# Performance work log

Measured on AMD Instinct MI355X. Metric: run time of the kernel, lower is better.

Reference implementation:

```python
import jax, jax.numpy as jnp
import numpy as np

NUM_LAYERS = 2
HIDDEN = 512


def setup_inputs() -> dict:
    key = jax.random.key(0)
    ks = jax.random.split(key, 5)
    B, T, D, L, H = 32, 512, 512, NUM_LAYERS, HIDDEN
    s = 1.0 / np.sqrt(H)
    return {
        "x": jax.random.normal(ks[0], (B, T, D), dtype=jnp.float32),
        "h0": jnp.zeros((B, L, H), dtype=jnp.float32),
        "c0": jnp.zeros((B, L, H), dtype=jnp.float32),
        "Wx": jax.random.normal(ks[1], (L, 4 * H, D), dtype=jnp.float32) * s,
        "bx": jax.random.normal(ks[2], (L, 4 * H), dtype=jnp.float32) * s,
        "Wh": jax.random.normal(ks[3], (L, 4 * H, H), dtype=jnp.float32) * s,
        "bh": jax.random.normal(ks[4], (L, 4 * H), dtype=jnp.float32) * s,
    }


def _lstm_forward(x, h0, c0, Wx, bx, Wh, bh):
    # x: [B,T,D]; h0,c0: [B,L,H]; Wx/Wh: [L,4H,*]; gate order (i,f,g,o)
    L, H = Wx.shape[0], Wx.shape[2]

    def step(carry, x_t):
        h, c = carry  # [B,L,H]
        inp = x_t  # [B,D]
        new_h, new_c = [], []
        for l in range(L):
            gates = (inp @ Wx[l].T + bx[l]) + (h[:, l] @ Wh[l].T + bh[l])  # [B,4H]
            i_g, f_g, g_g, o_g = jnp.split(gates, 4, axis=-1)
            c_l = jax.nn.sigmoid(f_g) * c[:, l] + jax.nn.sigmoid(i_g) * jnp.tanh(g_g)
            h_l = jax.nn.sigmoid(o_g) * jnp.tanh(c_l)
            new_h.append(h_l)
            new_c.append(c_l)
            inp = h_l
        return (jnp.stack(new_h, axis=1), jnp.stack(new_c, axis=1)), inp

    (h_n, c_n), ys = jax.lax.scan(step, (h0, c0), jnp.swapaxes(x, 0, 1))
    output = jnp.swapaxes(ys, 0, 1)  # [B,T,H]
    # torch module returns h_n/c_n swapped to [num_layers, batch, hidden]
    return output, (jnp.swapaxes(h_n, 0, 1), jnp.swapaxes(c_n, 0, 1))


def reference(x, h0, c0, Wx, bx, Wh, bh):
    return _lstm_forward(x, h0, c0, Wx, bx, Wh, bh)
```

## Files before the change

### kernel.cpp

```cpp
#include <hip/hip_runtime.h>
#include <hip/hip_bf16.h>

typedef __bf16 bf16x8 __attribute__((ext_vector_type(8)));
typedef float f32x4 __attribute__((ext_vector_type(4)));
typedef unsigned long long u64;

#define MFMA16(a, b, c) __builtin_amdgcn_mfma_f32_16x16x32_bf16((a), (b), (c), 0, 0, 0)

#define HN_OFF 8388608ull
#define CN_OFF 8421376ull

__device__ __forceinline__ float sigf(float x) { return 1.0f / (1.0f + __expf(-x)); }
__device__ __forceinline__ float b2f(unsigned short u) {
    union { unsigned u; float f; } c; c.u = ((unsigned)u) << 16; return c.f;
}
__device__ __forceinline__ unsigned short f2u(float f) {
    __hip_bfloat16 h = __float2bfloat16(f); return *(unsigned short*)&h;
}

__device__ __forceinline__ u64 gload8(const void* p) {
    return __hip_atomic_load((const u64*)p, __ATOMIC_RELAXED, __HIP_MEMORY_SCOPE_AGENT);
}
__device__ __forceinline__ void gstore8(void* p, u64 v) {
    __hip_atomic_store((u64*)p, v, __ATOMIC_RELAXED, __HIP_MEMORY_SCOPE_AGENT);
}

__device__ __forceinline__ void split8(const float* p, bf16x8& hi, bf16x8& lo) {
    union { __hip_bfloat16 h[8]; bf16x8 v; } uh, ul;
    #pragma unroll
    for (int i = 0; i < 8; ++i) {
        __hip_bfloat16 e = __float2bfloat16(p[i]);
        uh.h[i] = e;
        ul.h[i] = __float2bfloat16(p[i] - __bfloat162float(e));
    }
    hi = uh.v; lo = ul.v;
}

__global__ __launch_bounds__(256) void lstm_detect(
    const unsigned* __restrict__ Wq, unsigned* __restrict__ dflag,
    unsigned* __restrict__ flags)
{
    for (int j = threadIdx.x; j < 1024; j += 256) flags[j] = 0;
    if (threadIdx.x < 64) {
        int lane = threadIdx.x;
        int bad = 0;
        #pragma unroll
        for (int i = 0; i < 4; ++i) {
            unsigned u = Wq[(size_t)(lane + i * 64) * 4093];
            float v = b2f((unsigned short)(u & 0xFFFFu));
            if (!(v == v) || fabsf(v) > 100.0f) ++bad;
        }
        #pragma unroll
        for (int off = 32; off; off >>= 1) bad += __shfl_down(bad, off, 64);
        if (lane == 0) *dflag = (bad > 32) ? 1u : 0u;
    }
}

__global__ __launch_bounds__(256) void lstm_init(
    const void* __restrict__ h0v, const void* __restrict__ c0v,
    unsigned* __restrict__ h0p, unsigned* __restrict__ h1p,
    float* __restrict__ cws, const unsigned* __restrict__ dflag)
{
    const bool f32 = (*dflag != 0);
    int i = blockIdx.x * 256 + threadIdx.x;
    int b = i >> 9, n = i & 511;
    float f0, f1, g0, g1;
    if (f32) {
        const float* h = (const float*)h0v; const float* c = (const float*)c0v;
        f0 = h[(b * 2 + 0) * 512 + n];  f1 = h[(b * 2 + 1) * 512 + n];
        g0 = c[(b * 2 + 0) * 512 + n];  g1 = c[(b * 2 + 1) * 512 + n];
    } else {
        const unsigned short* h = (const unsigned short*)h0v;
        const unsigned short* c = (const unsigned short*)c0v;
        f0 = b2f(h[(b * 2 + 0) * 512 + n]);  f1 = b2f(h[(b * 2 + 1) * 512 + n]);
        g0 = b2f(c[(b * 2 + 0) * 512 + n]);  g1 = b2f(c[(b * 2 + 1) * 512 + n]);
    }
    unsigned short h0h = f2u(f0), h1h = f2u(f1);
    unsigned short h0l = f2u(f0 - b2f(h0h)), h1l = f2u(f1 - b2f(h1h));
    h0p[i] = ((unsigned)h0h << 16) | ((unsigned)h0l & 0xFFF0u) | 15u;
    h1p[i] = ((unsigned)h1h << 16) | ((unsigned)h1l & 0xFFF0u) | 0u;
    cws[i] = g0;  cws[16384 + i] = g1;
}

__global__ __launch_bounds__(256, 1) void lstm_seq(
    const void* __restrict__ xv,
    const void* __restrict__ Wxv, const void* __restrict__ bxv,
    const void* __restrict__ Whv, const void* __restrict__ bhv,
    unsigned* __restrict__ h0p, unsigned* __restrict__ h1p,
    const float* __restrict__ cws, unsigned* __restrict__ flags,
    const unsigned* __restrict__ dflag, void* __restrict__ outv)
{
    const bool f32 = (*dflag != 0);
    const int p  = blockIdx.x & 1;
    const int wt = blockIdx.x >> 1;
    const int tid = threadIdx.x;
    const int q = tid >> 6, lane = tid & 63;
    const int n16 = lane & 15, quad = lane >> 4;
    const int colg = q * 512 + wt * 16 + n16;

    __shared__ __align__(16) char smem[131072];
    __shared__ float gbuf[2176];

    float* outf = (float*)outv;
    __hip_bfloat16* outh = (__hip_bfloat16*)outv;

    bf16x8 wa[16], wal[16], wr[16], wrl[16];
    if (f32) {
        const float* WA = (const float*)Wxv + ((size_t)(p * 2048 + colg)) * 512;
        const float* WR = (const float*)Whv + ((size_t)(p * 2048 + colg)) * 512;
        #pragma unroll
        for (int kk = 0; kk < 16; ++kk) {
            split8(WA + kk * 32 + quad * 8, wa[kk], wal[kk]);
            split8(WR + kk * 32 + quad * 8, wr[kk], wrl[kk]);
        }
    } else {
        const unsigned short* WA = (const unsigned short*)Wxv + ((size_t)(p * 2048 + colg)) * 512;
        const unsigned short* WR = (const unsigned short*)Whv + ((size_t)(p * 2048 + colg)) * 512;
        union { uint4 u; bf16x8 v; } cvu;
        #pragma unroll
        for (int kk = 0; kk < 16; ++kk) {
            cvu.u = *(const uint4*)(WA + kk * 32 + quad * 8); wa[kk] = cvu.v;
            cvu.u = *(const uint4*)(WR + kk * 32 + quad * 8); wr[kk] = cvu.v;
        }
    }
    float bias;
    if (f32) bias = ((const float*)bxv)[p * 2048 + colg] + ((const float*)bhv)[p * 2048 + colg];
    else     bias = b2f(((const unsigned short*)bxv)[p * 2048 + colg])
                  + b2f(((const unsigned short*)bhv)[p * 2048 + colg]);

    const int e0 = tid * 2;
    const int pbb = e0 >> 4;
    const int pn0 = e0 & 15;
    float cv[2];
    cv[0] = cws[p * 16384 + pbb * 512 + wt * 16 + pn0];
    cv[1] = cws[p * 16384 + pbb * 512 + wt * 16 + pn0 + 1];

    const unsigned short* xb = (const unsigned short*)xv;

    #define STAGE_X_BF16(T)                                                      \
        { _Pragma("unroll")                                                      \
          for (int j = 0; j < 8; ++j) {                                          \
              int L = j * 256 + tid;                                             \
              int rem = L & 127;                                                 \
              int row = ((rem >> 6) << 4) + (rem & 15);                          \
              int kcol = ((L >> 7) << 5) + (((rem >> 4) & 3) << 3);              \
              *(uint4*)(smem + (L << 4)) =                                       \
                  *(const uint4*)(xb + ((size_t)row * 512 + (T)) * 512 + kcol);  \
          } }

    #define STAGE_X_F32(T)                                                       \
        { _Pragma("unroll")                                                      \
          for (int j = 0; j < 8; ++j) {                                          \
              int L = j * 256 + tid;                                             \
              int rem = L & 127;                                                 \
              int row = ((rem >> 6) << 4) + (rem & 15);                          \
              int kcol = ((L >> 7) << 5) + (((rem >> 4) & 3) << 3);              \
              const float* xp = (const float*)xv + ((size_t)row * 512 + (T)) * 512 + kcol; \
              bf16x8 hi_, lo_;                                                   \
              split8(xp, hi_, lo_);                                              \
              *(bf16x8*)(smem + (L << 4)) = hi_;                                 \
              *(bf16x8*)(smem + 32768 + (L << 4)) = lo_;                         \
          } }

    #define EOFF(S_) ({ int L_ = ((S_) >> 2) * 256 + tid; int rem_ = L_ & 127;    \
        int row_ = ((rem_ >> 6) << 4) + (rem_ & 15);                              \
        int kc_  = ((L_ >> 7) << 5) + (((rem_ >> 4) & 3) << 3);                   \
        row_ * 512 + kc_ + ((S_) & 3) * 2; })

    #define GISSUE(SRC)                                                           \
        { _Pragma("unroll")                                                       \
          for (int s_ = 0; s_ < 32; ++s_) V[s_] = gload8((const unsigned*)(SRC) + EOFF(s_)); }

    #define GCHECK(SRC, WANTV)                                                    \
        { const u64 WV_ = (u64)(WANTV) * 0x0000000100000001ULL;                   \
          for (;;) {                                                              \
              u64 d_ = 0;                                                         \
              _Pragma("unroll")                                                   \
              for (int s_ = 0; s_ < 32; ++s_)                                     \
                  d_ |= (V[s_] ^ WV_) & 0x0000000F0000000FULL;                    \
              if (d_ == 0) break;                                                 \
              __builtin_amdgcn_s_sleep(1);                                        \
              _Pragma("unroll")                                                   \
              for (int s_ = 0; s_ < 32; ++s_)                                     \
                  V[s_] = gload8((const unsigned*)(SRC) + EOFF(s_));              \
          } }

    #define GSCATTER(DH, DL)                                                      \
        { _Pragma("unroll")                                                       \
          for (int j_ = 0; j_ < 8; ++j_) {                                        \
              union { u64 q; unsigned w[2]; } a_, b_, c_, d_;                     \
              a_.q = V[j_*4+0]; b_.q = V[j_*4+1]; c_.q = V[j_*4+2]; d_.q = V[j_*4+3]; \
              uint4 hi_, lo_;                                                     \
              hi_.x = (a_.w[0] >> 16) | (a_.w[1] & 0xFFFF0000u);                  \
              hi_.y = (b_.w[0] >> 16) | (b_.w[1] & 0xFFFF0000u);                  \
              hi_.z = (c_.w[0] >> 16) | (c_.w[1] & 0xFFFF0000u);                  \
              hi_.w = (d_.w[0] >> 16) | (d_.w[1] & 0xFFFF0000u);                  \
              lo_.x = (a_.w[0] & 0xFFF0u) | ((a_.w[1] & 0xFFF0u) << 16);          \
              lo_.y = (b_.w[0] & 0xFFF0u) | ((b_.w[1] & 0xFFF0u) << 16);          \
              lo_.z = (c_.w[0] & 0xFFF0u) | ((c_.w[1] & 0xFFF0u) << 16);          \
              lo_.w = (d_.w[0] & 0xFFF0u) | ((d_.w[1] & 0xFFF0u) << 16);          \
              int L_ = j_ * 256 + tid;                                            \
              *(uint4*)(smem + (DH) + (L_ << 4)) = hi_;                           \
              *(uint4*)(smem + (DL) + (L_ << 4)) = lo_;                           \
          } }

    #define MM_A_F32()                                                           \
        { _Pragma("unroll")                                                      \
          for (int kk = 0; kk < 16; ++kk) {                                      \
              bf16x8 Aha = *(const bf16x8*)(sl + kk * 2048);                     \
              bf16x8 Ahb = *(const bf16x8*)(sl + kk * 2048 + 1024);              \
              bf16x8 Ala = *(const bf16x8*)(sl + 32768 + kk * 2048);             \
              bf16x8 Alb = *(const bf16x8*)(sl + 32768 + kk * 2048 + 1024);      \
              acc0 = MFMA16(Aha, wa[kk], acc0);  acc1 = MFMA16(Ahb, wa[kk], acc1);   \
              acc0 = MFMA16(Aha, wal[kk], acc0); acc1 = MFMA16(Ahb, wal[kk], acc1);  \
              acc0 = MFMA16(Ala, wa[kk], acc0);  acc1 = MFMA16(Alb, wa[kk], acc1);   \
          } }

    #define MM_R_F32()                                                           \
        { _Pragma("unroll")                                                      \
          for (int kk = 0; kk < 16; ++kk) {                                      \
              bf16x8 Rha = *(const bf16x8*)(sl + 65536 + kk * 2048);             \
              bf16x8 Rhb = *(const bf16x8*)(sl + 65536 + kk * 2048 + 1024);      \
              bf16x8 Rla = *(const bf16x8*)(sl + 98304 + kk * 2048);             \
              bf16x8 Rlb = *(const bf16x8*)(sl + 98304 + kk * 2048 + 1024);      \
              acc0 = MFMA16(Rha, wr[kk], acc0);  acc1 = MFMA16(Rhb, wr[kk], acc1);   \
              acc0 = MFMA16(Rha, wrl[kk], acc0); acc1 = MFMA16(Rhb, wrl[kk], acc1);  \
              acc0 = MFMA16(Rla, wr[kk], acc0);  acc1 = MFMA16(Rlb, wr[kk], acc1);   \
          } }

    #define MM_A_BF16_P0()                                                       \
        { _Pragma("unroll")                                                      \
          for (int kk = 0; kk < 16; ++kk) {                                      \
              bf16x8 Aha = *(const bf16x8*)(sl + kk * 2048);                     \
              bf16x8 Ahb = *(const bf16x8*)(sl + kk * 2048 + 1024);              \
              acc0 = MFMA16(Aha, wa[kk], acc0);  acc1 = MFMA16(Ahb, wa[kk], acc1);   \
          } }

    #define MM_A_BF16_P1()                                                       \
        { _Pragma("unroll")                                                      \
          for (int kk = 0; kk < 16; ++kk) {                                      \
              bf16x8 Aha = *(const bf16x8*)(sl + kk * 2048);                     \
              bf16x8 Ahb = *(const bf16x8*)(sl + kk * 2048 + 1024);              \
              bf16x8 Ala = *(const bf16x8*)(sl + 32768 + kk * 2048);             \
              bf16x8 Alb = *(const bf16x8*)(sl + 32768 + kk * 2048 + 1024);      \
              acc0 = MFMA16(Aha, wa[kk], acc0);  acc1 = MFMA16(Ahb, wa[kk], acc1);   \
              acc0 = MFMA16(Ala, wa[kk], acc0);  acc1 = MFMA16(Alb, wa[kk], acc1);   \
          } }

    #define MM_R_BF16()                                                          \
        { _Pragma("unroll")                                                      \
          for (int kk = 0; kk < 16; ++kk) {                                      \
              bf16x8 Rha = *(const bf16x8*)(sl + 65536 + kk * 2048);             \
              bf16x8 Rhb = *(const bf16x8*)(sl + 65536 + kk * 2048 + 1024);      \
              bf16x8 Rla = *(const bf16x8*)(sl + 98304 + kk * 2048);             \
              bf16x8 Rlb = *(const bf16x8*)(sl + 98304 + kk * 2048 + 1024);      \
              acc0 = MFMA16(Rha, wr[kk], acc0);  acc1 = MFMA16(Rhb, wr[kk], acc1);   \
              acc0 = MFMA16(Rla, wr[kk], acc0);  acc1 = MFMA16(Rlb, wr[kk], acc1);   \
          } }

    #define EPILOGUE(ODST, TG)                                                    \
        { _Pragma("unroll")                                                       \
          for (int r = 0; r < 4; ++r) {                                           \
              gbuf[(q * 32 + quad * 4 + r) * 17 + n16]      = acc0[r];            \
              gbuf[(q * 32 + 16 + quad * 4 + r) * 17 + n16] = acc1[r];            \
          } }

    const char* sl = smem + (lane << 4);

    if (p == 0) {
        if (f32) { STAGE_X_F32(0) } else { STAGE_X_BF16(0) }
        __syncthreads();

        for (int k = 0; k < 512; ++k) {
            const unsigned want = (unsigned)((k - 1) & 15);
            u64 V[32];
            const unsigned* h0src = h0p + (size_t)(k & 3) * 16384;

            GISSUE(h0src)
            f32x4 acc0 = {bias, bias, bias, bias};
            f32x4 acc1 = {bias, bias, bias, bias};
            if (f32) { MM_A_F32() } else { MM_A_BF16_P0() }
            GCHECK(h0src, want)
            GSCATTER(65536, 98304)
            __syncthreads();
            if (f32) { MM_R_F32() } else { MM_R_BF16() }

            EPILOGUE(,)
            if (k >= 3 && tid < 32) {
                while ((int)__hip_atomic_load(&flags[tid * 16],
                           __ATOMIC_RELAXED, __HIP_MEMORY_SCOPE_AGENT) < k - 2)
                    __builtin_amdgcn_s_sleep(2);
            }
            __syncthreads();

            float rh[2], rc[2];
            #pragma unroll
            for (int j = 0; j < 2; ++j) {
                int n = pn0 + j;
                float ig = gbuf[(0 * 32 + pbb) * 17 + n];
                float fg = gbuf[(1 * 32 + pbb) * 17 + n];
                float gg = gbuf[(2 * 32 + pbb) * 17 + n];
                float og = gbuf[(3 * 32 + pbb) * 17 + n];
                float cnew = sigf(fg) * cv[j] + sigf(ig) * tanhf(gg);
                cv[j] = cnew; rc[j] = cnew;
                rh[j] = sigf(og) * tanhf(cnew);
            }
            const unsigned tg = (unsigned)(k & 15);
            unsigned short hu0 = f2u(rh[0]), hu1 = f2u(rh[1]);
            unsigned short lu0 = f2u(rh[0] - b2f(hu0)), lu1 = f2u(rh[1] - b2f(hu1));
            unsigned w0 = ((unsigned)hu0 << 16) | ((unsigned)lu0 & 0xFFF0u) | tg;
            unsigned w1 = ((unsigned)hu1 << 16) | ((unsigned)lu1 & 0xFFF0u) | tg;
            const int idx = pbb * 512 + wt * 16 + pn0;
            gstore8(h0p + (size_t)((k + 1) & 3) * 16384 + idx, ((u64)w1 << 32) | w0);

            if (k == 511) {
                unsigned phi = (unsigned)hu0 | ((unsigned)hu1 << 16);
                unsigned pcn = (unsigned)f2u(rc[0]) | ((unsigned)f2u(rc[1]) << 16);
                if (f32) {
                    outf[HN_OFF + idx] = rh[0]; outf[HN_OFF + idx + 1] = rh[1];
                    outf[CN_OFF + idx] = rc[0]; outf[CN_OFF + idx + 1] = rc[1];
                } else {
                    *(unsigned*)(outh + HN_OFF + idx) = phi;
                    *(unsigned*)(outh + CN_OFF + idx) = pcn;
                }
            }
            if (k + 1 < 512) { if (f32) { STAGE_X_F32(k + 1) } else { STAGE_X_BF16(k + 1) } }
            __syncthreads();
        }
    } else {
        for (int k = 1; k <= 512; ++k) {
            const int t = k - 1;
            const unsigned want = (unsigned)((k - 1) & 15);
            u64 V[32];

            const unsigned* h1src = h1p + (size_t)((k + 1) & 1) * 16384;
            GISSUE(h1src)
            GCHECK(h1src, want)
            GSCATTER(65536, 98304)
            __syncthreads();

            const unsigned* h0src = h0p + (size_t)(k & 3) * 16384;
            GISSUE(h0src)
            f32x4 acc0 = {bias, bias, bias, bias};
            f32x4 acc1 = {bias, bias, bias, bias};
            if (f32) { MM_R_F32() } else { MM_R_BF16() }
            GCHECK(h0src, want)
            GSCATTER(0, 32768)
            __syncthreads();
            if (tid == 0)
                __hip_atomic_store(&flags[wt * 16], (unsigned)k,
                                   __ATOMIC_RELAXED, __HIP_MEMORY_SCOPE_AGENT);
            if (f32) { MM_A_F32() } else { MM_A_BF16_P1() }

            EPILOGUE(,)
            __syncthreads();

            float rh[2], rc[2];
            #pragma unroll
            for (int j = 0; j < 2; ++j) {
                int n = pn0 + j;
                float ig = gbuf[(0 * 32 + pbb) * 17 + n];
                float fg = gbuf[(1 * 32 + pbb) * 17 + n];
                float gg = gbuf[(2 * 32 + pbb) * 17 + n];
                float og = gbuf[(3 * 32 + pbb) * 17 + n];
                float cnew = sigf(fg) * cv[j] + sigf(ig) * tanhf(gg);
                cv[j] = cnew; rc[j] = cnew;
                rh[j] = sigf(og) * tanhf(cnew);
            }
            const unsigned tg = (unsigned)(k & 15);
            unsigned short hu0 = f2u(rh[0]), hu1 = f2u(rh[1]);
            unsigned short lu0 = f2u(rh[0] - b2f(hu0)), lu1 = f2u(rh[1] - b2f(hu1));
            unsigned w0 = ((unsigned)hu0 << 16) | ((unsigned)lu0 & 0xFFF0u) | tg;
            unsigned w1 = ((unsigned)hu1 << 16) | ((unsigned)lu1 & 0xFFF0u) | tg;
            const int idx = pbb * 512 + wt * 16 + pn0;
            gstore8(h1p + (size_t)(k & 1) * 16384 + idx, ((u64)w1 << 32) | w0);

            unsigned phi = (unsigned)hu0 | ((unsigned)hu1 << 16);
            size_t oidx = ((size_t)pbb * 512 + t) * 512 + wt * 16 + pn0;
            if (f32) { outf[oidx] = rh[0]; outf[oidx + 1] = rh[1]; }
            else     { *(unsigned*)(outh + oidx) = phi; }
            if (k == 512) {
                unsigned pcn = (unsigned)f2u(rc[0]) | ((unsigned)f2u(rc[1]) << 16);
                if (f32) {
                    outf[HN_OFF + 16384 + idx] = rh[0]; outf[HN_OFF + 16385 + idx] = rh[1];
                    outf[CN_OFF + 16384 + idx] = rc[0]; outf[CN_OFF + 16385 + idx] = rc[1];
                } else {
                    *(unsigned*)(outh + HN_OFF + 16384 + idx) = phi;
                    *(unsigned*)(outh + CN_OFF + 16384 + idx) = pcn;
                }
            }
        }
    }
}

extern "C" void kernel_launch(void* const* d_in, const int* in_sizes, int n_in,
                              void* d_out, int out_size, void* d_ws, size_t ws_size,
                              hipStream_t stream)
{
    const void* x  = d_in[0];
    const void* h0 = d_in[1];
    const void* c0 = d_in[2];
    const void* Wx = d_in[3];
    const void* bx = d_in[4];
    const void* Wh = d_in[5];
    const void* bh = d_in[6];

    char* ws = (char*)d_ws;
    unsigned* h0p  = (unsigned*)(ws);
    unsigned* h1p  = (unsigned*)(ws + 262144);
    float*    cws  = (float*)(ws + 393216);
    unsigned* flags = (unsigned*)(ws + 524288);
    unsigned* dflag = (unsigned*)(ws + 528384);

    lstm_detect<<<1, 256, 0, stream>>>((const unsigned*)Wx, dflag, flags);
    lstm_init<<<64, 256, 0, stream>>>(h0, c0, h0p, h1p, cws, dflag);
    lstm_seq<<<64, 256, 0, stream>>>(x, Wx, bx, Wh, bh,
                                     h0p, h1p, cws, flags, dflag, d_out);
}
```

Baseline: 7.190 ms.

## Software-pipeline LSTM layer loops so input GEMM precedes the hidden-state wait

Restructures both the layer-0 and layer-1 persistent loops so that the next step's input-projection GEMM and the spin-wait on the incoming hidden state run at the end of the current iteration, rather than at the start after a barrier. The flag wait in layer 0 moves after the pointwise math and right before the store, so it overlaps computation. The spin loops also skip s_sleep for the first few polls and drop sleep from the flag wait, to cut wake-up latency on the critical recurrent path. In exchange, busy polling uses more memory bandwidth and issue slots, and the reordered prologue and epilogue logic adds risk of tag or handshake mistakes.

```diff
diff --git a/kernel.cpp b/kernel.cpp
--- a/kernel.cpp
+++ b/kernel.cpp
@@ -173,13 +173,14 @@
 
     #define GCHECK(SRC, WANTV)                                                    \
         { const u64 WV_ = (u64)(WANTV) * 0x0000000100000001ULL;                   \
+          int it_ = 0;                                                            \
           for (;;) {                                                              \
               u64 d_ = 0;                                                         \
               _Pragma("unroll")                                                   \
               for (int s_ = 0; s_ < 32; ++s_)                                     \
                   d_ |= (V[s_] ^ WV_) & 0x0000000F0000000FULL;                    \
               if (d_ == 0) break;                                                 \
-              __builtin_amdgcn_s_sleep(1);                                        \
+              if (++it_ > 8) __builtin_amdgcn_s_sleep(1);                         \
               _Pragma("unroll")                                                   \
               for (int s_ = 0; s_ < 32; ++s_)                                     \
                   V[s_] = gload8((const unsigned*)(SRC) + EOFF(s_));              \
@@ -258,7 +259,21 @@
               acc0 = MFMA16(Rla, wr[kk], acc0);  acc1 = MFMA16(Rlb, wr[kk], acc1);   \
           } }
 
-    #define EPILOGUE(ODST, TG)                                                    \
+    #define POINTWISE()                                                           \
+        float rh[2], rc[2];                                                       \
+        { _Pragma("unroll")                                                       \
+          for (int j = 0; j < 2; ++j) {                                           \
+              int n = pn0 + j;                                                    \
+              float ig = gbuf[(0 * 32 + pbb) * 17 + n];                           \
+              float fg = gbuf[(1 * 32 + pbb) * 17 + n];                           \
+              float gg = gbuf[(2 * 32 + pbb) * 17 + n];                           \
+              float og = gbuf[(3 * 32 + pbb) * 17 + n];                           \
+              float cnew = sigf(fg) * cv[j] + sigf(ig) * tanhf(gg);               \
+              cv[j] = cnew; rc[j] = cnew;                                         \
+              rh[j] = sigf(og) * tanhf(cnew);                                     \
+          } }
+
+    #define GBUF_WR()                                                             \
         { _Pragma("unroll")                                                       \
           for (int r = 0; r < 4; ++r) {                                           \
               gbuf[(q * 32 + quad * 4 + r) * 17 + n16]      = acc0[r];            \
@@ -266,51 +281,34 @@
           } }
 
     const char* sl = smem + (lane << 4);
+    const int idx = pbb * 512 + wt * 16 + pn0;
+    u64 V[32];
+    f32x4 acc0, acc1;
 
     if (p == 0) {
         if (f32) { STAGE_X_F32(0) } else { STAGE_X_BF16(0) }
         __syncthreads();
+        acc0 = (f32x4){bias, bias, bias, bias}; acc1 = acc0;
+        if (f32) { MM_A_F32() } else { MM_A_BF16_P0() }
+        { const unsigned* s0 = h0p; GISSUE(s0) GCHECK(s0, 15u) }
 
         for (int k = 0; k < 512; ++k) {
-            const unsigned want = (unsigned)((k - 1) & 15);
-            u64 V[32];
-            const unsigned* h0src = h0p + (size_t)(k & 3) * 16384;
-
-            GISSUE(h0src)
-            f32x4 acc0 = {bias, bias, bias, bias};
-            f32x4 acc1 = {bias, bias, bias, bias};
-            if (f32) { MM_A_F32() } else { MM_A_BF16_P0() }
-            GCHECK(h0src, want)
             GSCATTER(65536, 98304)
             __syncthreads();
             if (f32) { MM_R_F32() } else { MM_R_BF16() }
-
-            EPILOGUE(,)
-            if (k >= 3 && tid < 32) {
-                while ((int)__hip_atomic_load(&flags[tid * 16],
-                           __ATOMIC_RELAXED, __HIP_MEMORY_SCOPE_AGENT) < k - 2)
-                    __builtin_amdgcn_s_sleep(2);
-            }
+            GBUF_WR()
             __syncthreads();
-
-            float rh[2], rc[2];
-            #pragma unroll
-            for (int j = 0; j < 2; ++j) {
-                int n = pn0 + j;
-                float ig = gbuf[(0 * 32 + pbb) * 17 + n];
-                float fg = gbuf[(1 * 32 + pbb) * 17 + n];
-                float gg = gbuf[(2 * 32 + pbb) * 17 + n];
-                float og = gbuf[(3 * 32 + pbb) * 17 + n];
-                float cnew = sigf(fg) * cv[j] + sigf(ig) * tanhf(gg);
-                cv[j] = cnew; rc[j] = cnew;
-                rh[j] = sigf(og) * tanhf(cnew);
-            }
+            POINTWISE()
             const unsigned tg = (unsigned)(k & 15);
             unsigned short hu0 = f2u(rh[0]), hu1 = f2u(rh[1]);
             unsigned short lu0 = f2u(rh[0] - b2f(hu0)), lu1 = f2u(rh[1] - b2f(hu1));
             unsigned w0 = ((unsigned)hu0 << 16) | ((unsigned)lu0 & 0xFFF0u) | tg;
             unsigned w1 = ((unsigned)hu1 << 16) | ((unsigned)lu1 & 0xFFF0u) | tg;
-            const int idx = pbb * 512 + wt * 16 + pn0;
+
+            if (k >= 3 && tid < 32) {
+                while ((int)__hip_atomic_load(&flags[tid * 16],
+                           __ATOMIC_RELAXED, __HIP_MEMORY_SCOPE_AGENT) < k - 2) {}
+            }
             gstore8(h0p + (size_t)((k + 1) & 3) * 16384 + idx, ((u64)w1 << 32) | w0);
 
             if (k == 511) {
@@ -323,60 +321,42 @@
                     *(unsigned*)(outh + HN_OFF + idx) = phi;
                     *(unsigned*)(outh + CN_OFF + idx) = pcn;
                 }
+            } else {
+                if (f32) { STAGE_X_F32(k + 1) } else { STAGE_X_BF16(k + 1) }
+                __syncthreads();
+                acc0 = (f32x4){bias, bias, bias, bias}; acc1 = acc0;
+                if (f32) { MM_A_F32() } else { MM_A_BF16_P0() }
+                const unsigned* h0src = h0p + (size_t)((k + 1) & 3) * 16384;
+                GISSUE(h0src) GCHECK(h0src, tg)
             }
-            if (k + 1 < 512) { if (f32) { STAGE_X_F32(k + 1) } else { STAGE_X_BF16(k + 1) } }
-            __syncthreads();
         }
     } else {
+        { const unsigned* s0 = h0p + 16384; GISSUE(s0) GCHECK(s0, 0u) }
+        GSCATTER(0, 32768)
+        __syncthreads();
+        if (tid == 0)
+            __hip_atomic_store(&flags[wt * 16], 1u,
+                               __ATOMIC_RELAXED, __HIP_MEMORY_SCOPE_AGENT);
+        acc0 = (f32x4){bias, bias, bias, bias}; acc1 = acc0;
+        if (f32) { MM_A_F32() } else { MM_A_BF16_P1() }
+        { const unsigned* s1 = h1p; GISSUE(s1) GCHECK(s1, 0u) }
+
         for (int k = 1; k <= 512; ++k) {
-            const int t = k - 1;
-            const unsigned want = (unsigned)((k - 1) & 15);
-            u64 V[32];
-
-            const unsigned* h1src = h1p + (size_t)((k + 1) & 1) * 16384;
-            GISSUE(h1src)
-            GCHECK(h1src, want)
             GSCATTER(65536, 98304)
             __syncthreads();
-
-            const unsigned* h0src = h0p + (size_t)(k & 3) * 16384;
-            GISSUE(h0src)
-            f32x4 acc0 = {bias, bias, bias, bias};
-            f32x4 acc1 = {bias, bias, bias, bias};
             if (f32) { MM_R_F32() } else { MM_R_BF16() }
-            GCHECK(h0src, want)
-            GSCATTER(0, 32768)
+            GBUF_WR()
             __syncthreads();
-            if (tid == 0)
-                __hip_atomic_store(&flags[wt * 16], (unsigned)k,
-                                   __ATOMIC_RELAXED, __HIP_MEMORY_SCOPE_AGENT);
-            if (f32) { MM_A_F32() } else { MM_A_BF16_P1() }
-
-            EPILOGUE(,)
-            __syncthreads();
-
-            float rh[2], rc[2];
-            #pragma unroll
-            for (int j = 0; j < 2; ++j) {
-                int n = pn0 + j;
-                float ig = gbuf[(0 * 32 + pbb) * 17 + n];
-                float fg = gbuf[(1 * 32 + pbb) * 17 + n];
-                float gg = gbuf[(2 * 32 + pbb) * 17 + n];
-                float og = gbuf[(3 * 32 + pbb) * 17 + n];
-                float cnew = sigf(fg) * cv[j] + sigf(ig) * tanhf(gg);
-                cv[j] = cnew; rc[j] = cnew;
-                rh[j] = sigf(og) * tanhf(cnew);
-            }
+            POINTWISE()
             const unsigned tg = (unsigned)(k & 15);
             unsigned short hu0 = f2u(rh[0]), hu1 = f2u(rh[1]);
             unsigned short lu0 = f2u(rh[0] - b2f(hu0)), lu1 = f2u(rh[1] - b2f(hu1));
             unsigned w0 = ((unsigned)hu0 << 16) | ((unsigned)lu0 & 0xFFF0u) | tg;
             unsigned w1 = ((unsigned)hu1 << 16) | ((unsigned)lu1 & 0xFFF0u) | tg;
-            const int idx = pbb * 512 + wt * 16 + pn0;
             gstore8(h1p + (size_t)(k & 1) * 16384 + idx, ((u64)w1 << 32) | w0);
 
             unsigned phi = (unsigned)hu0 | ((unsigned)hu1 << 16);
-            size_t oidx = ((size_t)pbb * 512 + t) * 512 + wt * 16 + pn0;
+            size_t oidx = ((size_t)pbb * 512 + (k - 1)) * 512 + wt * 16 + pn0;
             if (f32) { outf[oidx] = rh[0]; outf[oidx + 1] = rh[1]; }
             else     { *(unsigned*)(outh + oidx) = phi; }
             if (k == 512) {
@@ -388,6 +368,23 @@
                     *(unsigned*)(outh + HN_OFF + 16384 + idx) = phi;
                     *(unsigned*)(outh + CN_OFF + 16384 + idx) = pcn;
                 }
+                break;
+            }
+
+            {
+                const unsigned* h0src = h0p + (size_t)((k + 1) & 3) * 16384;
+                GISSUE(h0src) GCHECK(h0src, tg)
+            }
+            GSCATTER(0, 32768)
+            __syncthreads();
+            if (tid == 0)
+                __hip_atomic_store(&flags[wt * 16], (unsigned)(k + 1),
+                                   __ATOMIC_RELAXED, __HIP_MEMORY_SCOPE_AGENT);
+            acc0 = (f32x4){bias, bias, bias, bias}; acc1 = acc0;
+            if (f32) { MM_A_F32() } else { MM_A_BF16_P1() }
+            {
+                const unsigned* h1src = h1p + (size_t)(k & 1) * 16384;
+                GISSUE(h1src) GCHECK(h1src, tg)
             }
         }
     }
```

After: 6.693 ms. 1.07x faster.
